# Kernel optimization log

Hardware: AMD Instinct MI355X
Metric: run time of the kernel (lower is better)

Reference implementation:

```python
import jax, jax.numpy as jnp
import numpy as np

NFILT = 40          # mel filters
NBINS = 257         # nfft//2 + 1
HID = 64            # myconfig.LSTM_HIDDEN_SIZE
NLAYERS = 3         # myconfig.LSTM_NUM_LAYERS
B, T = 64, 2000


def setup_inputs() -> dict:
    key = jax.random.key(0)
    ks = jax.random.split(key, 16)
    x = jax.random.uniform(ks[0], (B, T, NBINS), jnp.float32)  # nonneg spectrogram-like
    # torch init: sorted randint(1, 257, (nfilt+2,)); sample w/o replacement -> distinct integer edges
    binpoints = jnp.sort(jax.random.permutation(ks[1], jnp.arange(1, 257))[:NFILT + 2]).astype(jnp.float32)
    s = 1.0 / np.sqrt(HID)
    def u(k, shape):
        return jax.random.uniform(k, shape, jnp.float32, -s, s)
    inp = {"x": x, "binpoints": binpoints}
    in_sizes = [NFILT, 2 * HID, 2 * HID]
    for l in range(NLAYERS):
        inp[f"w_ih_{l}"] = u(ks[2 + 4 * l], (2, 4 * HID, in_sizes[l]))
        inp[f"w_hh_{l}"] = u(ks[3 + 4 * l], (2, 4 * HID, HID))
        inp[f"b_ih_{l}"] = u(ks[4 + 4 * l], (2, 4 * HID))
        inp[f"b_hh_{l}"] = u(ks[5 + 4 * l], (2, 4 * HID))
    return inp


def make_fbank(binpoints):
    """Vectorized version of the torch double loop (one pass of broadcasted comparisons)."""
    b = jnp.sort(binpoints)                       # (42,)
    bj, bj1, bj2 = b[:NFILT], b[1:NFILT + 1], b[2:NFILT + 2]
    fb = jnp.floor(b)                             # int() truncation in torch loop bounds
    i = jnp.arange(NBINS, dtype=b.dtype)[None, :]  # (1, 257)
    rise_m = (i >= fb[:NFILT, None]) & (i < fb[1:NFILT + 1, None])
    fall_m = (i >= fb[1:NFILT + 1, None]) & (i < fb[2:NFILT + 2, None])
    d1 = bj1 - bj
    d2 = bj2 - bj1
    rise_v = (i - bj[:, None]) / jnp.where(d1 > 0, d1, 1.0)[:, None] ** 2
    fall_v = (bj2[:, None] - i) / jnp.where(d2 > 0, d2, 1.0)[:, None] ** 2
    fbank = jnp.where(fall_m, fall_v, jnp.where(rise_m, rise_v, 0.0))
    # torch loop runs j in range(nfilt-1): last filter row never written
    fbank = fbank * (jnp.arange(NFILT) < NFILT - 1)[:, None]
    return fbank


def lstm_dir(x, w_ih, w_hh, b_ih, b_hh, reverse):
    xs = jnp.flip(x, 1) if reverse else x
    pre = jnp.einsum('btd,gd->btg', xs, w_ih) + b_ih + b_hh  # (B, T, 4H)
    h0 = jnp.zeros((x.shape[0], HID), x.dtype)

    def step(carry, p):
        h, c = carry
        g = p + h @ w_hh.T
        ig, fg, gg, og = jnp.split(g, 4, axis=-1)  # torch gate order i,f,g,o
        c = jax.nn.sigmoid(fg) * c + jax.nn.sigmoid(ig) * jnp.tanh(gg)
        h = jax.nn.sigmoid(og) * jnp.tanh(c)
        return (h, c), h

    _, ys = jax.lax.scan(step, (h0, h0), jnp.swapaxes(pre, 0, 1))
    ys = jnp.swapaxes(ys, 0, 1)  # (B, T, H)
    return jnp.flip(ys, 1) if reverse else ys


def reference(x, binpoints, w_ih_0, w_hh_0, b_ih_0, b_hh_0,
              w_ih_1, w_hh_1, b_ih_1, b_hh_1,
              w_ih_2, w_hh_2, b_ih_2, b_hh_2):
    fbank = make_fbank(binpoints)                       # (40, 257)
    filt = jnp.einsum('btn,fn->btf', x, fbank)          # x @ fbank.T
    filt = filt.at[:, :, 0].set(x[:, :, 0])             # keep first column
    # remove_zero_rows is an identity here: no frame has an all-zero feature sum
    h = jnp.log(filt + 1e-10)
    params = [(w_ih_0, w_hh_0, b_ih_0, b_hh_0),
              (w_ih_1, w_hh_1, b_ih_1, b_hh_1),
              (w_ih_2, w_hh_2, b_ih_2, b_hh_2)]
    for (wi, wh, bi, bh) in params:  # bidirectional, 3 layers
        fwd = lstm_dir(h, wi[0], wh[0], bi[0], bh[0], False)
        bwd = lstm_dir(h, wi[1], wh[1], bi[1], bh[1], True)
        h = jnp.concatenate([fwd, bwd], axis=-1)        # (B, T, 2H)
    return jnp.mean(h, axis=1)                          # FRAME_AGGREGATION_MEAN
```

## Files before the change

kernel.cpp:

```cpp
#include <hip/hip_runtime.h>
#include <cstdint>
#include <cstddef>

#define NFILT 40
#define NBINS 257
#define HID   64
#define BB    64
#define TT    2000
#define GATES 256
#define MTOT  (BB*TT)

typedef float float2v __attribute__((ext_vector_type(2)));
typedef float float4v __attribute__((ext_vector_type(4)));

__device__ __forceinline__ float2v pk_fma(float2v a, float2v b, float2v c) {
  asm("v_pk_fma_f32 %0, %1, %2, %0" : "+v"(c) : "v"(a), "v"(b));
  return c;
}
__device__ __forceinline__ float2v pk_fma_bl(float2v h2, float2v w2, float2v c) {
  asm("v_pk_fma_f32 %0, %1, %2, %0 op_sel:[0,0,0] op_sel_hi:[0,1,1]"
      : "+v"(c) : "v"(h2), "v"(w2));
  return c;
}
__device__ __forceinline__ float2v pk_fma_bh(float2v h2, float2v w2, float2v c) {
  asm("v_pk_fma_f32 %0, %1, %2, %0 op_sel:[1,0,0] op_sel_hi:[1,1,1]"
      : "+v"(c) : "v"(h2), "v"(w2));
  return c;
}

__device__ __forceinline__ float sigm(float x) {
  return 1.0f / (1.0f + __expf(-x));
}

__device__ __forceinline__ float bfly1(float x) {
  int i = __builtin_amdgcn_mov_dpp(__float_as_int(x), 0xB1, 0xF, 0xF, true);
  return x + __int_as_float(i);
}
__device__ __forceinline__ float bfly2(float x) {
  int i = __builtin_amdgcn_mov_dpp(__float_as_int(x), 0x4E, 0xF, 0xF, true);
  return x + __int_as_float(i);
}
#define QB(x, ctrl) __int_as_float(__builtin_amdgcn_mov_dpp(__float_as_int(x), (ctrl), 0xF, 0xF, true))

__global__ void k_fbank(const float* __restrict__ binpoints,
                        float* __restrict__ fbank,
                        int* __restrict__ lohi ) {
  __shared__ float b[NFILT + 2];
  int tid = threadIdx.x;
  if (tid < NFILT + 2) b[tid] = binpoints[tid];
  __syncthreads();
  if (tid < NFILT) {
    if (tid == NFILT - 1) { lohi[tid] = 0; lohi[NFILT + tid] = 0; }
    else {
      int lo = (int)floorf(b[tid]);
      int hi = (int)floorf(b[tid + 2]);
      if (lo < 0) lo = 0;
      if (hi > NBINS) hi = NBINS;
      lohi[tid] = lo; lohi[NFILT + tid] = hi;
    }
  }
  for (int idx = tid; idx < NFILT * NBINS; idx += blockDim.x) {
    int f = idx / NBINS, i = idx - f * NBINS;
    float bj = b[f], bj1 = b[f + 1], bj2 = b[f + 2];
    float fb0 = floorf(bj), fb1 = floorf(bj1), fb2 = floorf(bj2);
    float fi = (float)i;
    bool rise = (fi >= fb0) && (fi < fb1);
    bool fall = (fi >= fb1) && (fi < fb2);
    float d1 = bj1 - bj;  d1 = (d1 > 0.f) ? d1 : 1.f;
    float d2 = bj2 - bj1; d2 = (d2 > 0.f) ? d2 : 1.f;
    float rv = (fi - bj)  / (d1 * d1);
    float fv = (bj2 - fi) / (d2 * d2);
    float v = fall ? fv : (rise ? rv : 0.f);
    if (f == NFILT - 1) v = 0.f;
    fbank[idx] = v;
  }
}

__global__ __launch_bounds__(256) void k_feat(const float* __restrict__ x,
                                              const float* __restrict__ fbank,
                                              const int* __restrict__ lohi,
                                              float* __restrict__ h0) {
  const int wv   = threadIdx.x >> 6;
  const int lane = threadIdx.x & 63;
  const int bt   = blockIdx.x * 4 + wv;
  __shared__ float xs[4][NBINS];
  const float* xr = x + (size_t)bt * NBINS;
  for (int i = lane; i < NBINS; i += 64) xs[wv][i] = xr[i];
  __syncthreads();
  if (lane < NFILT) {
    float acc = 0.f;
    int lo = lohi[lane], hi = lohi[NFILT + lane];
    for (int i = lo; i < hi; ++i) acc = fmaf(xs[wv][i], fbank[lane * NBINS + i], acc);
    float val = (lane == 0) ? xs[wv][0] : acc;
    h0[(size_t)bt * NFILT + lane] = logf(val + 1e-10f);
  }
}

template <int K, int BK>
__global__ __launch_bounds__(256) void k_gemm(const float* __restrict__ Hm,
                                              const float* __restrict__ W,
                                              const float* __restrict__ bih,
                                              const float* __restrict__ bhh,
                                              float* __restrict__ pre) {
  constexpr int BM = 128, BN = 64;
  __shared__ float Hs[BK][BM + 4];
  __shared__ float Ws[BK][BN + 4];
  const int d  = blockIdx.z;
  const int m0 = blockIdx.x * BM;
  const int g0 = blockIdx.y * BN;
  const int tid = threadIdx.x;
  const int tx = tid & 15, ty = tid >> 4;

  float2v acc2[8][2];
#pragma unroll
  for (int r = 0; r < 8; ++r) {
    acc2[r][0] = (float2v){0.f, 0.f};
    acc2[r][1] = (float2v){0.f, 0.f};
  }

  for (int k0 = 0; k0 < K; k0 += BK) {
    constexpr int HE4 = BM * BK / 4;
#pragma unroll
    for (int i = 0; i < (HE4 + 255) / 256; ++i) {
      int f4 = tid + i * 256;
      if ((HE4 % 256 == 0) || (f4 < HE4)) {
        int e = f4 * 4, r = e / BK, kk = e - r * BK;
        const float4 v = *(const float4*)&Hm[(size_t)(m0 + r) * K + k0 + kk];
        Hs[kk][r] = v.x; Hs[kk + 1][r] = v.y; Hs[kk + 2][r] = v.z; Hs[kk + 3][r] = v.w;
      }
    }
    constexpr int WE4 = BN * BK / 4;
#pragma unroll
    for (int i = 0; i < (WE4 + 255) / 256; ++i) {
      int f4 = tid + i * 256;
      if ((WE4 % 256 == 0) || (f4 < WE4)) {
        int e = f4 * 4, r = e / BK, kk = e - r * BK;
        const float4 v = *(const float4*)&W[((size_t)d * GATES + g0 + r) * K + k0 + kk];
        Ws[kk][r] = v.x; Ws[kk + 1][r] = v.y; Ws[kk + 2][r] = v.z; Ws[kk + 3][r] = v.w;
      }
    }
    __syncthreads();
#pragma unroll
    for (int kk = 0; kk < BK; ++kk) {
      const float4v wv  = *(const float4v*)&Ws[kk][tx * 4];
      const float4v hv0 = *(const float4v*)&Hs[kk][ty * 8];
      const float4v hv1 = *(const float4v*)&Hs[kk][ty * 8 + 4];
      const float2v w01 = __builtin_shufflevector(wv, wv, 0, 1);
      const float2v w23 = __builtin_shufflevector(wv, wv, 2, 3);
      float2v hp[4];
      hp[0] = __builtin_shufflevector(hv0, hv0, 0, 1);
      hp[1] = __builtin_shufflevector(hv0, hv0, 2, 3);
      hp[2] = __builtin_shufflevector(hv1, hv1, 0, 1);
      hp[3] = __builtin_shufflevector(hv1, hv1, 2, 3);
#pragma unroll
      for (int rp = 0; rp < 4; ++rp) {
        acc2[2 * rp + 0][0] = pk_fma_bl(hp[rp], w01, acc2[2 * rp + 0][0]);
        acc2[2 * rp + 0][1] = pk_fma_bl(hp[rp], w23, acc2[2 * rp + 0][1]);
        acc2[2 * rp + 1][0] = pk_fma_bh(hp[rp], w01, acc2[2 * rp + 1][0]);
        acc2[2 * rp + 1][1] = pk_fma_bh(hp[rp], w23, acc2[2 * rp + 1][1]);
      }
    }
    __syncthreads();
  }

  const int gcol = g0 + tx * 4;
  const float4 bi = *(const float4*)&bih[d * GATES + gcol];
  const float4 bh = *(const float4*)&bhh[d * GATES + gcol];
  const float bx = bi.x + bh.x, by = bi.y + bh.y, bz = bi.z + bh.z, bw = bi.w + bh.w;
#pragma unroll
  for (int r = 0; r < 8; ++r) {
    size_t m = (size_t)(m0 + ty * 8 + r);
    float4 o = {acc2[r][0].x + bx, acc2[r][0].y + by, acc2[r][1].x + bz, acc2[r][1].y + bw};
    *(float4*)&pre[((size_t)d * MTOT + m) * GATES + gcol] = o;
  }
}

__global__ __attribute__((amdgpu_waves_per_eu(1, 1)))
__launch_bounds__(256) void k_lstmq(const float* __restrict__ pre,
                                    const float* __restrict__ whh,
                                    float* __restrict__ hout,
                                    float* __restrict__ out,
                                    int final_layer) {
  const int b   = blockIdx.x;
  const int d   = blockIdx.y;
  const int tid = threadIdx.x;
  const int wl  = tid >> 6;
  const int l   = tid & 63;
  const int uu  = wl * 16 + (l >> 2);
  const int p   = l & 3;
  const int p16 = p * 16;

  __shared__ __align__(16) float hs[2][HID];

  float2v wp[4][8];
#pragma unroll
  for (int q = 0; q < 4; ++q) {
    const float4* wr = (const float4*)(whh + ((size_t)d * GATES + q * HID + uu) * HID + p16);
#pragma unroll
    for (int c2 = 0; c2 < 4; ++c2) {
      const float4 t4 = wr[c2];
      wp[q][2 * c2].x     = t4.x; wp[q][2 * c2].y     = t4.y;
      wp[q][2 * c2 + 1].x = t4.z; wp[q][2 * c2 + 1].y = t4.w;
    }
  }
#pragma unroll
  for (int q = 0; q < 4; ++q)
#pragma unroll
    for (int i = 0; i < 8; ++i) asm volatile("" : "+v"(wp[q][i]));

  const float sA = (p == 2) ? 2.f : 1.f;
  const float aA = (p == 2) ? 2.f : 1.f;
  const float aB = (p == 2) ? -1.f : 0.f;
  const bool  p1 = (p & 1) != 0;
  const bool  p2 = (p & 2) != 0;

  if (tid < HID) { hs[0][tid] = 0.f; hs[1][tid] = 0.f; }
  float c = 0.f, sum = 0.f;
  __syncthreads();

  const int t0 = d ? (TT - 1) : 0;
  const int dt = d ? -1 : 1;
  const float* pp = pre + ((size_t)d * MTOT + (size_t)b * TT + t0) * GATES + (p * HID + uu);
  const ptrdiff_t pstr = (ptrdiff_t)dt * GATES;

  float pf0 = pp[0], pf1 = pp[pstr], pf2 = pp[pstr * 2], pf3 = pp[pstr * 3];

#define GDOT(Q)                                                                 \
  ({ float2v acc_ = {0.f, 0.f};                                                 \
     acc_ = pk_fma(A0, wp[Q][0], acc_);                                         \
     acc_ = pk_fma(A1, wp[Q][1], acc_);                                         \
     acc_ = pk_fma(B0, wp[Q][2], acc_);                                         \
     acc_ = pk_fma(B1, wp[Q][3], acc_);                                         \
     acc_ = pk_fma(C0, wp[Q][4], acc_);                                         \
     acc_ = pk_fma(C1, wp[Q][5], acc_);                                         \
     acc_ = pk_fma(D0, wp[Q][6], acc_);                                         \
     acc_ = pk_fma(D1, wp[Q][7], acc_);                                         \
     acc_.x + acc_.y; })

#define LSTM_STEP(TK, PAR, PF)                                                  \
  do {                                                                          \
    const float4* h4 = (const float4*)&hs[PAR][p16];                            \
    const float4 hA = h4[0], hB = h4[1], hC = h4[2], hD = h4[3];                \
    float2v A0, A1, B0, B1, C0, C1, D0, D1;                                     \
    A0.x = hA.x; A0.y = hA.y; A1.x = hA.z; A1.y = hA.w;                         \
    B0.x = hB.x; B0.y = hB.y; B1.x = hB.z; B1.y = hB.w;                         \
    C0.x = hC.x; C0.y = hC.y; C1.x = hC.z; C1.y = hC.w;                         \
    D0.x = hD.x; D0.y = hD.y; D1.x = hD.z; D1.y = hD.w;                         \
    float a0 = GDOT(0);                                                         \
    float a1 = GDOT(1);                                                         \
    float a2 = GDOT(2);                                                         \
    float a3 = GDOT(3);                                                         \
    a0 = bfly2(bfly1(a0)); a1 = bfly2(bfly1(a1));                               \
    a2 = bfly2(bfly1(a2)); a3 = bfly2(bfly1(a3));                               \
    const float t02 = p2 ? a2 : a0;                                             \
    const float t13 = p2 ? a3 : a1;                                             \
    const float zsel = (p1 ? t13 : t02) + (PF);                                 \
    const float act = fmaf(sigm(zsel * sA), aA, aB);                            \
    const float ig = QB(act, 0x00), fg = QB(act, 0x55);                         \
    const float gg = QB(act, 0xAA), og = QB(act, 0xFF);                         \
    c = fmaf(fg, c, ig * gg);                                                   \
    const float tc = fmaf(sigm(2.f * c), 2.f, -1.f);                            \
    const float hvv = og * tc;                                                  \
    if (p == 0) hs[(PAR) ^ 1][uu] = hvv;                                        \
    asm volatile("s_waitcnt lgkmcnt(0)\n\ts_barrier" ::: "memory");             \
    if (final_layer) sum += hvv;                                                \
    else if (p == 0)                                                            \
      hout[((size_t)b * TT + (size_t)(t0 + dt * (TK))) * (2 * HID) + d * HID + uu] = hvv; \
  } while (0)

  for (int t = 0; t < TT; t += 4) {
    LSTM_STEP(t + 0, 0, pf0);
    { int ip = t + 4; if (ip >= TT) ip = 0; pf0 = pp[pstr * (ptrdiff_t)ip]; }
    LSTM_STEP(t + 1, 1, pf1);
    { int ip = t + 5; if (ip >= TT) ip = 0; pf1 = pp[pstr * (ptrdiff_t)ip]; }
    LSTM_STEP(t + 2, 0, pf2);
    { int ip = t + 6; if (ip >= TT) ip = 0; pf2 = pp[pstr * (ptrdiff_t)ip]; }
    LSTM_STEP(t + 3, 1, pf3);
    { int ip = t + 7; if (ip >= TT) ip = 0; pf3 = pp[pstr * (ptrdiff_t)ip]; }
  }
#undef LSTM_STEP
#undef GDOT

  if (final_layer && p == 0) out[b * (2 * HID) + d * HID + uu] = sum * (1.0f / (float)TT);
}

extern "C" void kernel_launch(void* const* d_in, const int* in_sizes, int n_in,
                              void* d_out, int out_size, void* d_ws, size_t ws_size,
                              hipStream_t stream) {
  const float* x         = (const float*)d_in[0];
  const float* binpoints = (const float*)d_in[1];
  const float* w_ih[3] = {(const float*)d_in[2], (const float*)d_in[6],  (const float*)d_in[10]};
  const float* w_hh[3] = {(const float*)d_in[3], (const float*)d_in[7],  (const float*)d_in[11]};
  const float* b_ih[3] = {(const float*)d_in[4], (const float*)d_in[8],  (const float*)d_in[12]};
  const float* b_hh[3] = {(const float*)d_in[5], (const float*)d_in[9],  (const float*)d_in[13]};
  float* out = (float*)d_out;

  float* pre   = (float*)d_ws;
  float* Hbuf  = pre  + (size_t)2 * MTOT * GATES;
  float* h0    = Hbuf + (size_t)MTOT * 128;
  float* fbank = h0   + (size_t)MTOT * NFILT;
  int*   lohi  = (int*)(fbank + NFILT * NBINS);

  k_fbank<<<1, 256, 0, stream>>>(binpoints, fbank, lohi);
  k_feat<<<MTOT / 4, 256, 0, stream>>>(x, fbank, lohi, h0);

  k_gemm<40, 40><<<dim3(MTOT / 128, GATES / 64, 2), 256, 0, stream>>>(h0, w_ih[0], b_ih[0], b_hh[0], pre);
  k_lstmq<<<dim3(BB, 2), 256, 0, stream>>>(pre, w_hh[0], Hbuf, out, 0);

  k_gemm<128, 32><<<dim3(MTOT / 128, GATES / 64, 2), 256, 0, stream>>>(Hbuf, w_ih[1], b_ih[1], b_hh[1], pre);
  k_lstmq<<<dim3(BB, 2), 256, 0, stream>>>(pre, w_hh[1], Hbuf, out, 0);

  k_gemm<128, 32><<<dim3(MTOT / 128, GATES / 64, 2), 256, 0, stream>>>(Hbuf, w_ih[2], b_ih[2], b_hh[2], pre);
  k_lstmq<<<dim3(BB, 2), 256, 0, stream>>>(pre, w_hh[2], Hbuf, out, 1);
}
```

Before: 2.824 ms.

## Run LSTM recurrence in a single wavefront with fp16 dot2 weights

Replaces the 4-wave LSTM recurrence kernel with a single 64-lane wave per (batch, direction). Each lane owns one hidden unit and computes all four gate dot products itself, using fp16 weights held in registers and v_dot2 instructions. The input-projection GEMM permutes gate columns so each lane can load its four gates as one float4, and the block barrier, DPP reductions and gate broadcasts are removed. The cost is fp16 rounding of h and W_hh in the recurrence, plus a serial per-lane dot product of length 64.

```diff
diff --git a/kernel.cpp b/kernel.cpp
--- a/kernel.cpp
+++ b/kernel.cpp
@@ -10,13 +10,16 @@
 #define GATES 256
 #define MTOT  (BB*TT)
 
-typedef float float2v __attribute__((ext_vector_type(2)));
-typedef float float4v __attribute__((ext_vector_type(4)));
-
-__device__ __forceinline__ float2v pk_fma(float2v a, float2v b, float2v c) {
-  asm("v_pk_fma_f32 %0, %1, %2, %0" : "+v"(c) : "v"(a), "v"(b));
-  return c;
-}
+typedef float   float2v __attribute__((ext_vector_type(2)));
+typedef float   float4v __attribute__((ext_vector_type(4)));
+typedef _Float16 half2v __attribute__((ext_vector_type(2)));
+typedef _Float16 half8v __attribute__((ext_vector_type(8)));
+
+__device__ __forceinline__ float fdot2_(half2v a, half2v b, float c) {
+  return __builtin_amdgcn_fdot2(a, b, c, false);
+}
+#define SH2(HB, m) __builtin_shufflevector(HB, HB, 2 * (m), 2 * (m) + 1)
+
 __device__ __forceinline__ float2v pk_fma_bl(float2v h2, float2v w2, float2v c) {
   asm("v_pk_fma_f32 %0, %1, %2, %0 op_sel:[0,0,0] op_sel_hi:[0,1,1]"
       : "+v"(c) : "v"(h2), "v"(w2));
@@ -31,16 +34,13 @@
 __device__ __forceinline__ float sigm(float x) {
   return 1.0f / (1.0f + __expf(-x));
 }
-
-__device__ __forceinline__ float bfly1(float x) {
-  int i = __builtin_amdgcn_mov_dpp(__float_as_int(x), 0xB1, 0xF, 0xF, true);
-  return x + __int_as_float(i);
-}
-__device__ __forceinline__ float bfly2(float x) {
-  int i = __builtin_amdgcn_mov_dpp(__float_as_int(x), 0x4E, 0xF, 0xF, true);
-  return x + __int_as_float(i);
-}
-#define QB(x, ctrl) __int_as_float(__builtin_amdgcn_mov_dpp(__float_as_int(x), (ctrl), 0xF, 0xF, true))
+__device__ __forceinline__ float tanh_(float x) {
+  float e = __expf(-2.0f * fabsf(x));
+  float r = (1.0f - e) / (1.0f + e);
+  return copysignf(r, x);
+}
+
+__device__ __forceinline__ int gperm(int gp) { return ((gp & 3) << 6) | (gp >> 2); }
 
 __global__ void k_fbank(const float* __restrict__ binpoints,
                         float* __restrict__ fbank,
@@ -135,7 +135,7 @@
       int f4 = tid + i * 256;
       if ((WE4 % 256 == 0) || (f4 < WE4)) {
         int e = f4 * 4, r = e / BK, kk = e - r * BK;
-        const float4 v = *(const float4*)&W[((size_t)d * GATES + g0 + r) * K + k0 + kk];
+        const float4 v = *(const float4*)&W[((size_t)d * GATES + gperm(g0 + r)) * K + k0 + kk];
         Ws[kk][r] = v.x; Ws[kk + 1][r] = v.y; Ws[kk + 2][r] = v.z; Ws[kk + 3][r] = v.w;
       }
     }
@@ -164,124 +164,111 @@
   }
 
   const int gcol = g0 + tx * 4;
-  const float4 bi = *(const float4*)&bih[d * GATES + gcol];
-  const float4 bh = *(const float4*)&bhh[d * GATES + gcol];
-  const float bx = bi.x + bh.x, by = bi.y + bh.y, bz = bi.z + bh.z, bw = bi.w + bh.w;
+  float bsum[4];
+#pragma unroll
+  for (int i = 0; i < 4; ++i) {
+    const int og = gperm(gcol + i);
+    bsum[i] = bih[d * GATES + og] + bhh[d * GATES + og];
+  }
 #pragma unroll
   for (int r = 0; r < 8; ++r) {
     size_t m = (size_t)(m0 + ty * 8 + r);
-    float4 o = {acc2[r][0].x + bx, acc2[r][0].y + by, acc2[r][1].x + bz, acc2[r][1].y + bw};
+    float4 o = {acc2[r][0].x + bsum[0], acc2[r][0].y + bsum[1],
+                acc2[r][1].x + bsum[2], acc2[r][1].y + bsum[3]};
     *(float4*)&pre[((size_t)d * MTOT + m) * GATES + gcol] = o;
   }
 }
 
 __global__ __attribute__((amdgpu_waves_per_eu(1, 1)))
-__launch_bounds__(256) void k_lstmq(const float* __restrict__ pre,
+__launch_bounds__(64) void k_lstm1w(const float* __restrict__ pre,
                                     const float* __restrict__ whh,
                                     float* __restrict__ hout,
                                     float* __restrict__ out,
                                     int final_layer) {
-  const int b   = blockIdx.x;
-  const int d   = blockIdx.y;
-  const int tid = threadIdx.x;
-  const int wl  = tid >> 6;
-  const int l   = tid & 63;
-  const int uu  = wl * 16 + (l >> 2);
-  const int p   = l & 3;
-  const int p16 = p * 16;
-
-  __shared__ __align__(16) float hs[2][HID];
-
-  float2v wp[4][8];
+  const int b = blockIdx.x & (BB - 1);
+  const int d = blockIdx.x >> 6;
+  const int j = threadIdx.x;
+  __shared__ __align__(16) _Float16 hs16[HID];
+
+  half2v wq[4][32];
 #pragma unroll
   for (int q = 0; q < 4; ++q) {
-    const float4* wr = (const float4*)(whh + ((size_t)d * GATES + q * HID + uu) * HID + p16);
-#pragma unroll
-    for (int c2 = 0; c2 < 4; ++c2) {
+    const float4* wr = (const float4*)(whh + ((size_t)d * GATES + q * HID + j) * HID);
+#pragma unroll
+    for (int c2 = 0; c2 < 16; ++c2) {
       const float4 t4 = wr[c2];
-      wp[q][2 * c2].x     = t4.x; wp[q][2 * c2].y     = t4.y;
-      wp[q][2 * c2 + 1].x = t4.z; wp[q][2 * c2 + 1].y = t4.w;
+      wq[q][2 * c2]     = (half2v){(_Float16)t4.x, (_Float16)t4.y};
+      wq[q][2 * c2 + 1] = (half2v){(_Float16)t4.z, (_Float16)t4.w};
     }
   }
 #pragma unroll
   for (int q = 0; q < 4; ++q)
 #pragma unroll
-    for (int i = 0; i < 8; ++i) asm volatile("" : "+v"(wp[q][i]));
-
-  const float sA = (p == 2) ? 2.f : 1.f;
-  const float aA = (p == 2) ? 2.f : 1.f;
-  const float aB = (p == 2) ? -1.f : 0.f;
-  const bool  p1 = (p & 1) != 0;
-  const bool  p2 = (p & 2) != 0;
-
-  if (tid < HID) { hs[0][tid] = 0.f; hs[1][tid] = 0.f; }
+    for (int i = 0; i < 32; ++i) asm volatile("" : "+v"(wq[q][i]));
+
+  hs16[j] = (_Float16)0.f;
   float c = 0.f, sum = 0.f;
-  __syncthreads();
+  __builtin_amdgcn_wave_barrier();
 
   const int t0 = d ? (TT - 1) : 0;
   const int dt = d ? -1 : 1;
-  const float* pp = pre + ((size_t)d * MTOT + (size_t)b * TT + t0) * GATES + (p * HID + uu);
-  const ptrdiff_t pstr = (ptrdiff_t)dt * GATES;
-
-  float pf0 = pp[0], pf1 = pp[pstr], pf2 = pp[pstr * 2], pf3 = pp[pstr * 3];
-
-#define GDOT(Q)                                                                 \
-  ({ float2v acc_ = {0.f, 0.f};                                                 \
-     acc_ = pk_fma(A0, wp[Q][0], acc_);                                         \
-     acc_ = pk_fma(A1, wp[Q][1], acc_);                                         \
-     acc_ = pk_fma(B0, wp[Q][2], acc_);                                         \
-     acc_ = pk_fma(B1, wp[Q][3], acc_);                                         \
-     acc_ = pk_fma(C0, wp[Q][4], acc_);                                         \
-     acc_ = pk_fma(C1, wp[Q][5], acc_);                                         \
-     acc_ = pk_fma(D0, wp[Q][6], acc_);                                         \
-     acc_ = pk_fma(D1, wp[Q][7], acc_);                                         \
-     acc_.x + acc_.y; })
-
-#define LSTM_STEP(TK, PAR, PF)                                                  \
+  const float4* prow = (const float4*)pre;
+  const float4* pp = prow + ((size_t)d * MTOT + (size_t)b * TT + (size_t)t0) * 64 + j;
+  const ptrdiff_t pstr = (ptrdiff_t)dt * 64;
+
+  float4 pf0 = pp[0], pf1 = pp[pstr], pf2 = pp[pstr * 2], pf3 = pp[pstr * 3];
+
+#define DOTB(HB, K0)                                                            \
+    z0 = fdot2_(SH2(HB, 0), wq[0][(K0) + 0], z0);                               \
+    z1 = fdot2_(SH2(HB, 0), wq[1][(K0) + 0], z1);                               \
+    z2 = fdot2_(SH2(HB, 0), wq[2][(K0) + 0], z2);                               \
+    z3 = fdot2_(SH2(HB, 0), wq[3][(K0) + 0], z3);                               \
+    z0 = fdot2_(SH2(HB, 1), wq[0][(K0) + 1], z0);                               \
+    z1 = fdot2_(SH2(HB, 1), wq[1][(K0) + 1], z1);                               \
+    z2 = fdot2_(SH2(HB, 1), wq[2][(K0) + 1], z2);                               \
+    z3 = fdot2_(SH2(HB, 1), wq[3][(K0) + 1], z3);                               \
+    z0 = fdot2_(SH2(HB, 2), wq[0][(K0) + 2], z0);                               \
+    z1 = fdot2_(SH2(HB, 2), wq[1][(K0) + 2], z1);                               \
+    z2 = fdot2_(SH2(HB, 2), wq[2][(K0) + 2], z2);                               \
+    z3 = fdot2_(SH2(HB, 2), wq[3][(K0) + 2], z3);                               \
+    z0 = fdot2_(SH2(HB, 3), wq[0][(K0) + 3], z0);                               \
+    z1 = fdot2_(SH2(HB, 3), wq[1][(K0) + 3], z1);                               \
+    z2 = fdot2_(SH2(HB, 3), wq[2][(K0) + 3], z2);                               \
+    z3 = fdot2_(SH2(HB, 3), wq[3][(K0) + 3], z3);
+
+#define LSTM_STEP(TK, PF)                                                       \
   do {                                                                          \
-    const float4* h4 = (const float4*)&hs[PAR][p16];                            \
-    const float4 hA = h4[0], hB = h4[1], hC = h4[2], hD = h4[3];                \
-    float2v A0, A1, B0, B1, C0, C1, D0, D1;                                     \
-    A0.x = hA.x; A0.y = hA.y; A1.x = hA.z; A1.y = hA.w;                         \
-    B0.x = hB.x; B0.y = hB.y; B1.x = hB.z; B1.y = hB.w;                         \
-    C0.x = hC.x; C0.y = hC.y; C1.x = hC.z; C1.y = hC.w;                         \
-    D0.x = hD.x; D0.y = hD.y; D1.x = hD.z; D1.y = hD.w;                         \
-    float a0 = GDOT(0);                                                         \
-    float a1 = GDOT(1);                                                         \
-    float a2 = GDOT(2);                                                         \
-    float a3 = GDOT(3);                                                         \
-    a0 = bfly2(bfly1(a0)); a1 = bfly2(bfly1(a1));                               \
-    a2 = bfly2(bfly1(a2)); a3 = bfly2(bfly1(a3));                               \
-    const float t02 = p2 ? a2 : a0;                                             \
-    const float t13 = p2 ? a3 : a1;                                             \
-    const float zsel = (p1 ? t13 : t02) + (PF);                                 \
-    const float act = fmaf(sigm(zsel * sA), aA, aB);                            \
-    const float ig = QB(act, 0x00), fg = QB(act, 0x55);                         \
-    const float gg = QB(act, 0xAA), og = QB(act, 0xFF);                         \
+    __builtin_amdgcn_wave_barrier();   \
+    const half8v* h8p = (const half8v*)hs16;                                    \
+    const half8v hb0 = h8p[0], hb1 = h8p[1], hb2 = h8p[2], hb3 = h8p[3];        \
+    const half8v hb4 = h8p[4], hb5 = h8p[5], hb6 = h8p[6], hb7 = h8p[7];        \
+    float z0 = (PF).x, z1 = (PF).y, z2 = (PF).z, z3 = (PF).w;                   \
+    DOTB(hb0, 0)  DOTB(hb1, 4)  DOTB(hb2, 8)  DOTB(hb3, 12)                     \
+    DOTB(hb4, 16) DOTB(hb5, 20) DOTB(hb6, 24) DOTB(hb7, 28)                     \
+    const float ig = sigm(z0), fg = sigm(z1), gg = tanh_(z2), og = sigm(z3);    \
     c = fmaf(fg, c, ig * gg);                                                   \
-    const float tc = fmaf(sigm(2.f * c), 2.f, -1.f);                            \
-    const float hvv = og * tc;                                                  \
-    if (p == 0) hs[(PAR) ^ 1][uu] = hvv;                                        \
-    asm volatile("s_waitcnt lgkmcnt(0)\n\ts_barrier" ::: "memory");             \
+    const float hvv = og * tanh_(c);                                            \
+    __builtin_amdgcn_wave_barrier();   \
+    hs16[j] = (_Float16)hvv;                                                    \
     if (final_layer) sum += hvv;                                                \
-    else if (p == 0)                                                            \
-      hout[((size_t)b * TT + (size_t)(t0 + dt * (TK))) * (2 * HID) + d * HID + uu] = hvv; \
+    else                                                                        \
+      hout[((size_t)b * TT + (size_t)(t0 + dt * (TK))) * (2 * HID) + d * HID + j] = hvv; \
   } while (0)
 
   for (int t = 0; t < TT; t += 4) {
-    LSTM_STEP(t + 0, 0, pf0);
+    LSTM_STEP(t + 0, pf0);
     { int ip = t + 4; if (ip >= TT) ip = 0; pf0 = pp[pstr * (ptrdiff_t)ip]; }
-    LSTM_STEP(t + 1, 1, pf1);
+    LSTM_STEP(t + 1, pf1);
     { int ip = t + 5; if (ip >= TT) ip = 0; pf1 = pp[pstr * (ptrdiff_t)ip]; }
-    LSTM_STEP(t + 2, 0, pf2);
+    LSTM_STEP(t + 2, pf2);
     { int ip = t + 6; if (ip >= TT) ip = 0; pf2 = pp[pstr * (ptrdiff_t)ip]; }
-    LSTM_STEP(t + 3, 1, pf3);
+    LSTM_STEP(t + 3, pf3);
     { int ip = t + 7; if (ip >= TT) ip = 0; pf3 = pp[pstr * (ptrdiff_t)ip]; }
   }
 #undef LSTM_STEP
-#undef GDOT
-
-  if (final_layer && p == 0) out[b * (2 * HID) + d * HID + uu] = sum * (1.0f / (float)TT);
+#undef DOTB
+
+  if (final_layer) out[b * (2 * HID) + d * HID + j] = sum * (1.0f / (float)TT);
 }
 
 extern "C" void kernel_launch(void* const* d_in, const int* in_sizes, int n_in,
@@ -305,11 +292,11 @@
   k_feat<<<MTOT / 4, 256, 0, stream>>>(x, fbank, lohi, h0);
 
   k_gemm<40, 40><<<dim3(MTOT / 128, GATES / 64, 2), 256, 0, stream>>>(h0, w_ih[0], b_ih[0], b_hh[0], pre);
-  k_lstmq<<<dim3(BB, 2), 256, 0, stream>>>(pre, w_hh[0], Hbuf, out, 0);
+  k_lstm1w<<<BB * 2, 64, 0, stream>>>(pre, w_hh[0], Hbuf, out, 0);
 
   k_gemm<128, 32><<<dim3(MTOT / 128, GATES / 64, 2), 256, 0, stream>>>(Hbuf, w_ih[1], b_ih[1], b_hh[1], pre);
-  k_lstmq<<<dim3(BB, 2), 256, 0, stream>>>(pre, w_hh[1], Hbuf, out, 0);
+  k_lstm1w<<<BB * 2, 64, 0, stream>>>(pre, w_hh[1], Hbuf, out, 0);
 
   k_gemm<128, 32><<<dim3(MTOT / 128, GATES / 64, 2), 256, 0, stream>>>(Hbuf, w_ih[2], b_ih[2], b_hh[2], pre);
-  k_lstmq<<<dim3(BB, 2), 256, 0, stream>>>(pre, w_hh[2], Hbuf, out, 1);
-}
+  k_lstm1w<<<BB * 2, 64, 0, stream>>>(pre, w_hh[2], Hbuf, out, 1);
+}
```

After: 3.457 ms. +22.4%, slower.
